# Performance work log

Hardware: AMD Instinct MI355X
Metric: run time of the kernel (lower is better)

Reference implementation:

```python
import jax, jax.numpy as jnp
import numpy as np

# ---- static config (mirrors module init / config constants) ----
STATE_DIM = 512
D_H = 2048
INPUT_DIM = 1024
N_QUBITS = 6
N_VQC_LAYERS = 3
MSD = 128                 # mamba_state_dim (last dim of padded state)
PAD_SLICES = 16           # padded slice count in h_padded
MIN_T = 1e-6              # control_limits.min_value
REL_STEP = 0.1            # control_limits.hardware_relative_step
ABS_STEP = 1e-4           # control_limits.hardware_absolute_step
MAX_T = 0.05              # control_limits.max_value
DIM = 2 ** N_QUBITS

# qubit 0 = most significant bit (matches reshape-based gate application)
_BITS = ((np.arange(DIM)[:, None] >> np.arange(N_QUBITS)[None, ::-1]) & 1).astype(np.float32)
_sign = np.ones(DIM, np.float32)
for k in range(N_QUBITS):  # ring CZ entanglement
    k2 = (k + 1) % N_QUBITS
    _sign *= 1.0 - 2.0 * _BITS[:, k] * _BITS[:, k2]
CZ_SIGN = jnp.asarray(_sign)
Z_OBS = jnp.asarray((1.0 - 2.0 * _BITS).mean(axis=1))  # mean <Z_k> observable weights


def _apply_ry(state, ang, k):
    # state: [B, 2^n] real statevector; ang: [B] rotation angle on qubit k
    B = state.shape[0]
    s = state.reshape(B, 2 ** k, 2, 2 ** (N_QUBITS - k - 1))
    c = jnp.cos(ang / 2)[:, None, None]
    si = jnp.sin(ang / 2)[:, None, None]
    a0, a1 = s[:, :, 0, :], s[:, :, 1, :]
    out = jnp.stack([c * a0 - si * a1, si * a0 + c * a1], axis=2)
    return out.reshape(B, DIM)


def _vqc(feats, enc_W, enc_b, thetas):
    # EvolutionTimeVQCLayer: angle-encode features, layered RY + ring CZ, mean-Z expectation
    B = feats.shape[0]
    angles = feats @ enc_W + enc_b  # [B, n_qubits]
    state = jnp.zeros((B, DIM), feats.dtype).at[:, 0].set(1.0)
    for k in range(N_QUBITS):
        state = _apply_ry(state, angles[:, k], k)
    for l in range(N_VQC_LAYERS):
        for k in range(N_QUBITS):
            state = _apply_ry(state, jnp.broadcast_to(thetas[l, k], (B,)), k)
        state = state * CZ_SIGN[None, :]
    return (state * state) @ Z_OBS  # [B]


def _hamiltonian(q, p, x, W1, b1, W2, b2, W3, b3):
    z = jnp.concatenate([q, p, x], axis=-1)          # [B, 2*S + D]
    h1 = jnp.tanh(z @ W1 + b1)
    h2 = jnp.tanh(h1 @ W2 + b2)
    return (h2 @ W3)[:, 0] + b3                       # [B] scalar energy per sample


def setup_inputs() -> dict:
    key = jax.random.key(0)
    ks = jax.random.split(key, 12)
    def glorot(k, shape):
        std = np.sqrt(2.0 / (shape[0] + shape[-1]))
        return jax.random.normal(k, shape, jnp.float32) * std
    B = 2048
    h_in = 2 * STATE_DIM + INPUT_DIM
    gen_in = INPUT_DIM + 2 * STATE_DIM
    return {
        'x': jax.random.normal(ks[0], (B, INPUT_DIM), jnp.float32),
        'h_padded': jax.random.normal(ks[1], (B, PAD_SLICES, MSD), jnp.float32),
        'aux_padded': jnp.zeros((B, PAD_SLICES, MSD), jnp.float32),
        'W1': glorot(ks[2], (h_in, D_H)), 'b1': jnp.zeros((D_H,), jnp.float32),
        'W2': glorot(ks[3], (D_H, D_H)), 'b2': jnp.zeros((D_H,), jnp.float32),
        'W3': glorot(ks[4], (D_H, 1)), 'b3': jnp.zeros((), jnp.float32),
        'W_out': glorot(ks[5], (2 * STATE_DIM, INPUT_DIM)),
        'b_out': jnp.zeros((INPUT_DIM,), jnp.float32),
        'enc_W': glorot(ks[6], (gen_in, N_QUBITS)) * 0.1,
        'enc_b': jnp.zeros((N_QUBITS,), jnp.float32),
        'thetas': jax.random.normal(ks[7], (N_VQC_LAYERS, N_QUBITS), jnp.float32) * 0.1,
        'gain': jnp.asarray(0.1, jnp.float32),
        'shift': jnp.asarray(7.0, jnp.float32),
        'cap_param': jnp.asarray(0.02, jnp.float32),
        'time_bias': jnp.asarray(0.0005, jnp.float32),
        'last_stable': jnp.asarray(0.0005, jnp.float32),
    }


def reference(x, h_padded, aux_padded, W1, b1, W2, b2, W3, b3, W_out, b_out,
              enc_W, enc_b, thetas, gain, shift, cap_param, time_bias, last_stable):
    B = x.shape[0]
    total = 2 * STATE_DIM
    num_slices = total // MSD
    # unpack phase-space state from padded mamba-shaped state
    unpacked = h_padded[:, :num_slices, :].reshape(B, total)
    q_t, p_t = jnp.split(unpacked, 2, axis=-1)

    # ---- evolution-time generation via VQC ----
    ctrl = jnp.concatenate([x, q_t, p_t], axis=-1)
    samples = _vqc(ctrl, enc_W, enc_b, thetas)                       # [B]
    soft_gain = jax.nn.softplus(gain)
    soft_shift = jax.nn.softplus(shift)
    adjusted = jax.nn.softplus(soft_gain * samples - soft_shift)
    raw = jnp.mean(adjusted) + time_bias
    cap = jnp.maximum(jax.nn.softplus(cap_param), 1e-6)
    evo = cap * jax.nn.sigmoid(raw / cap)
    evo = jnp.where(jnp.isfinite(evo), evo, cap * jax.nn.sigmoid(time_bias / cap))
    prev = jnp.maximum(last_stable, MIN_T)
    cand = jnp.maximum(evo, MIN_T)
    max_step = jnp.maximum(prev * REL_STEP, ABS_STEP)
    cand = jnp.minimum(cand, prev + max_step)
    cand = jnp.minimum(cand, MAX_T)
    dt = jnp.where(jnp.isfinite(cand), cand, prev)                   # scalar

    # ---- fused HNN symplectic (leapfrog) step ----
    def H_sum(q, p):
        return _hamiltonian(q, p, x, W1, b1, W2, b2, W3, b3).sum()
    grad_qp = jax.grad(H_sum, argnums=(0, 1))
    dHdq0, _ = grad_qp(q_t, p_t)
    p_half = p_t - 0.5 * dt * dHdq0
    _, dHdp_h = grad_qp(q_t, p_half)
    q_next = q_t + dt * dHdp_h
    dHdq_n, _ = grad_qp(q_next, p_half)
    p_next = p_half - 0.5 * dt * dHdq_n

    out = jnp.concatenate([q_next, p_next], axis=-1) @ W_out + b_out  # [B, INPUT_DIM]

    # repack state into padded mamba layout
    new_slices = jnp.concatenate([q_next, p_next], axis=-1).reshape(B, num_slices, MSD)
    pad = jnp.zeros((B, PAD_SLICES - num_slices, MSD), out.dtype)
    h_next = jnp.concatenate([new_slices, pad], axis=1)
    return out, h_next
```

## Files before the change

### kernel.cpp

```cpp
#include <hip/hip_runtime.h>
#include <math.h>

#define NB 2048
#define ZD 2048
#define SD 512
#define NELEM_Z (NB * ZD)
#define MB_ (1024 * 1024)

typedef float f32x4 __attribute__((ext_vector_type(4)));
typedef __bf16 bf16x8 __attribute__((ext_vector_type(8)));
typedef __bf16 bf16x4 __attribute__((ext_vector_type(4)));
typedef int i32x4 __attribute__((ext_vector_type(4)));
typedef int i32x8 __attribute__((ext_vector_type(8)));
typedef long long i64;

__device__ __forceinline__ float softplus_f(float x) {
  if (x > 20.f) return x;
  if (x < -20.f) return expf(x);
  return log1pf(expf(x));
}

__device__ __forceinline__ void gload_lds16(const __bf16* g, __bf16* l) {
  __builtin_amdgcn_global_load_lds(
      (__attribute__((address_space(1))) void*)(g),
      (__attribute__((address_space(3))) void*)(l), 16, 0, 0);
}

__device__ __forceinline__ int pack_fp8x4(float a, float b, float c, float d) {
  int p = __builtin_amdgcn_cvt_pk_fp8_f32(a, b, 0, false);
  p = __builtin_amdgcn_cvt_pk_fp8_f32(c, d, p, true);
  return p;
}
__device__ __forceinline__ float fp8_to_f32(unsigned char b) {
  return __builtin_amdgcn_cvt_f32_fp8((int)b, 0);
}

__global__ __launch_bounds__(256) void build_z_kernel(
    const float* __restrict__ x,
    const float* __restrict__ h_padded,
    const float* __restrict__ enc_W,
    const float* __restrict__ enc_b,
    float* __restrict__ z,
    __bf16* __restrict__ zb,
    unsigned char* __restrict__ zf8,
    float* __restrict__ angles,
    float* __restrict__ acc) {
  int b = blockIdx.x;
  int tid = threadIdx.x;
  if (b == 0 && tid == 0) acc[0] = 0.f;
  int lane = tid & 63, w = tid >> 6;
  __shared__ float red[4][6];

  float pa[6] = {0.f, 0.f, 0.f, 0.f, 0.f, 0.f};
#pragma unroll
  for (int cc = 0; cc < 2; cc++) {
    int c = cc * 256 + tid;
    int i = c * 4;
    f32x4 v = (i < 1024) ? ((const f32x4*)(h_padded + (size_t)b * 2048))[c]
                         : ((const f32x4*)(x + (size_t)b * 1024))[c - 256];
    size_t zi = (size_t)b * 512 + c;
    ((f32x4*)z)[zi] = v;
    bf16x4 o;
    o[0] = (__bf16)v[0]; o[1] = (__bf16)v[1];
    o[2] = (__bf16)v[2]; o[3] = (__bf16)v[3];
    ((bf16x4*)zb)[zi] = o;
    ((int*)zf8)[zi] = pack_fp8x4(v[0], v[1], v[2], v[3]);
    int cj = (i < 1024) ? (1024 + i) : (i - 1024);
#pragma unroll
    for (int e = 0; e < 4; e++) {
      const float* wp = enc_W + (size_t)(cj + e) * 6;
#pragma unroll
      for (int k = 0; k < 6; k++) pa[k] += v[e] * wp[k];
    }
  }
#pragma unroll
  for (int k = 0; k < 6; k++)
    for (int off = 32; off > 0; off >>= 1) pa[k] += __shfl_down(pa[k], off, 64);
  if (lane == 0) {
#pragma unroll
    for (int k = 0; k < 6; k++) red[w][k] = pa[k];
  }
  __syncthreads();
  if (tid < 6)
    angles[b * 6 + tid] =
        red[0][tid] + red[1][tid] + red[2][tid] + red[3][tid] + enc_b[tid];
}

__global__ void prep_w(const float* __restrict__ in,
                       __bf16* __restrict__ outT, int R, int C) {
  __shared__ float tile[32][33];
  int bx = blockIdx.x * 32, by = blockIdx.y * 32;
  int tx = threadIdx.x, ty = threadIdx.y;
  for (int r = ty; r < 32; r += 8)
    tile[r][tx] = in[(size_t)(by + r) * C + bx + tx];
  __syncthreads();
  for (int r = ty; r < 32; r += 8)
    outT[(size_t)(bx + r) * R + by + tx] = (__bf16)tile[tx][r];
}

__global__ void prep_w8(const float* __restrict__ in,
                        unsigned char* __restrict__ outN,
                        unsigned char* __restrict__ outT, int R, int C) {
  __shared__ float tile[32][33];
  int bx = blockIdx.x * 32, by = blockIdx.y * 32;
  int tx = threadIdx.x, ty = threadIdx.y;
  for (int r = ty; r < 32; r += 8) {
    float v = in[(size_t)(by + r) * C + bx + tx] * 16.f;
    tile[r][tx] = v;
    int p = __builtin_amdgcn_cvt_pk_fp8_f32(v, v, 0, false);
    outN[(size_t)(by + r) * C + bx + tx] = (unsigned char)(p & 0xff);
  }
  __syncthreads();
  for (int r = ty; r < 32; r += 8) {
    float v = tile[tx][r];
    int p = __builtin_amdgcn_cvt_pk_fp8_f32(v, v, 0, false);
    outT[(size_t)(bx + r) * R + by + tx] = (unsigned char)(p & 0xff);
  }
}

__global__ __launch_bounds__(64) void sim_kernel(
    const float* __restrict__ angles,
    const float* __restrict__ thetas,
    const float* __restrict__ gain,
    const float* __restrict__ shift,
    float* __restrict__ acc) {
  int row = blockIdx.x * 64 + threadIdx.x;
  const float* a = angles + row * 6;

  float s[64];
#pragma unroll
  for (int i = 0; i < 64; i++) s[i] = 0.f;
  s[0] = 1.f;

#pragma unroll
  for (int k = 0; k < 6; k++) {
    float half = 0.5f * a[k];
    float c = cosf(half), si = sinf(half);
    int m = 1 << (5 - k);
#pragma unroll
    for (int i = 0; i < 64; i++) {
      if ((i & m) == 0) {
        float a0 = s[i], a1 = s[i | m];
        s[i] = c * a0 - si * a1;
        s[i | m] = si * a0 + c * a1;
      }
    }
  }
#pragma unroll
  for (int l = 0; l < 3; l++) {
#pragma unroll
    for (int k = 0; k < 6; k++) {
      float half = 0.5f * thetas[l * 6 + k];
      float c = cosf(half), si = sinf(half);
      int m = 1 << (5 - k);
#pragma unroll
      for (int i = 0; i < 64; i++) {
        if ((i & m) == 0) {
          float a0 = s[i], a1 = s[i | m];
          s[i] = c * a0 - si * a1;
          s[i | m] = si * a0 + c * a1;
        }
      }
    }
#pragma unroll
    for (int i = 0; i < 64; i++) {
      int rot = ((i << 1) | (i >> 5)) & 63;
      if (__popc(i & rot) & 1) s[i] = -s[i];
    }
  }

  float val = 0.f;
#pragma unroll
  for (int i = 0; i < 64; i++) {
    float zo = (6.f - 2.f * (float)__popc(i)) * (1.f / 6.f);
    val += s[i] * s[i] * zo;
  }
  float sg = softplus_f(gain[0]);
  float ss = softplus_f(shift[0]);
  float adj = softplus_f(sg * val - ss);
  for (int off = 32; off > 0; off >>= 1) adj += __shfl_down(adj, off, 64);
  if (threadIdx.x == 0) atomicAdd(acc, adj);
}

__global__ void dt_kernel(const float* __restrict__ acc,
                          const float* __restrict__ cap_param,
                          const float* __restrict__ time_bias,
                          const float* __restrict__ last_stable,
                          float* __restrict__ dt_out) {
  float raw = acc[0] * (1.f / (float)NB) + time_bias[0];
  float cap = fmaxf(softplus_f(cap_param[0]), 1e-6f);
  float evo = cap / (1.f + expf(-raw / cap));
  if (!isfinite(evo)) evo = cap / (1.f + expf(-time_bias[0] / cap));
  float prev = fmaxf(last_stable[0], 1e-6f);
  float cand = fmaxf(evo, 1e-6f);
  float max_step = fmaxf(prev * 0.1f, 1e-4f);
  cand = fminf(cand, prev + max_step);
  cand = fminf(cand, 0.05f);
  dt_out[0] = isfinite(cand) ? cand : prev;
}

template <int EPI>
__global__ __launch_bounds__(256, 2) void mfma_gemm8(
    const unsigned char* __restrict__ A, int lda,
    const unsigned char* __restrict__ Bt, int ldb,
    void* __restrict__ Cv, int ldc,
    const float* __restrict__ bias,
    const float* __restrict__ w3,
    const unsigned char* __restrict__ aux, int ldaux,
    int Kslice) {
  __shared__ __align__(16) unsigned char sA[2][128 * 128];
  __shared__ __align__(16) unsigned char sB[2][64 * 128];

  const int tid = threadIdx.x;
  const int lane = tid & 63;
  const int w = tid >> 6;
  const int wm = w & 1, wn = w >> 1;
  const int row0 = blockIdx.y * 128;
  const int col0 = blockIdx.x * 64;
  const int koff = blockIdx.z * Kslice;

  const unsigned char* gA[4]; int wA[4];
  const unsigned char* gB[2]; int wB[2];
#pragma unroll
  for (int i = 0; i < 4; i++) {
    int c = i * 256 + tid;
    int m = c >> 3, s = c & 7;
    gA[i] = A + (size_t)(row0 + m) * lda + koff + s * 16;
    wA[i] = m * 128 + ((s ^ (m & 7)) << 4);
  }
#pragma unroll
  for (int i = 0; i < 2; i++) {
    int c = i * 256 + tid;
    int m = c >> 3, s = c & 7;
    gB[i] = Bt + (size_t)(col0 + m) * ldb + koff + s * 16;
    wB[i] = m * 128 + ((s ^ (m & 7)) << 4);
  }

  const int q = lane >> 4, r = lane & 15;
  int aoff[4][2], boff[2][2];
#pragma unroll
  for (int i = 0; i < 4; i++) {
    int ma = wm * 64 + i * 16 + r;
#pragma unroll
    for (int H = 0; H < 2; H++)
      aoff[i][H] = ma * 128 + (((2 * q + H) ^ (ma & 7)) << 4);
  }
#pragma unroll
  for (int j = 0; j < 2; j++) {
    int mb = wn * 32 + j * 16 + r;
#pragma unroll
    for (int H = 0; H < 2; H++)
      boff[j][H] = mb * 128 + (((2 * q + H) ^ (mb & 7)) << 4);
  }

  f32x4 acc[4][2] = {};
  f32x4 rA[4], rB[2];

#pragma unroll
  for (int i = 0; i < 4; i++) rA[i] = *(const f32x4*)gA[i];
#pragma unroll
  for (int i = 0; i < 2; i++) rB[i] = *(const f32x4*)gB[i];
#pragma unroll
  for (int i = 0; i < 4; i++) *(f32x4*)(&sA[0][0] + wA[i]) = rA[i];
#pragma unroll
  for (int i = 0; i < 2; i++) *(f32x4*)(&sB[0][0] + wB[i]) = rB[i];
  __syncthreads();

  int cur = 0;
  for (int k0 = 0; k0 < Kslice; k0 += 128) {
    const bool more = (k0 + 128 < Kslice);
    if (more) {
#pragma unroll
      for (int i = 0; i < 4; i++) rA[i] = *(const f32x4*)(gA[i] + k0 + 128);
#pragma unroll
      for (int i = 0; i < 2; i++) rB[i] = *(const f32x4*)(gB[i] + k0 + 128);
    }

    const unsigned char* bA = &sA[cur][0];
    const unsigned char* bB = &sB[cur][0];
    i32x8 af[4], bfr[2];
#pragma unroll
    for (int i = 0; i < 4; i++) {
      i32x4 lo = *(const i32x4*)(bA + aoff[i][0]);
      i32x4 hi = *(const i32x4*)(bA + aoff[i][1]);
      af[i] = __builtin_shufflevector(lo, hi, 0, 1, 2, 3, 4, 5, 6, 7);
    }
#pragma unroll
    for (int j = 0; j < 2; j++) {
      i32x4 lo = *(const i32x4*)(bB + boff[j][0]);
      i32x4 hi = *(const i32x4*)(bB + boff[j][1]);
      bfr[j] = __builtin_shufflevector(lo, hi, 0, 1, 2, 3, 4, 5, 6, 7);
    }
#pragma unroll
    for (int i = 0; i < 4; i++)
#pragma unroll
      for (int j = 0; j < 2; j++)
        acc[i][j] = __builtin_amdgcn_mfma_scale_f32_16x16x128_f8f6f4(
            af[i], bfr[j], acc[i][j], 0 , 0 ,
            0, 0x7F7F7F7F, 0, 0x7F7F7F7F);

    if (more) {
      unsigned char* nA = &sA[cur ^ 1][0];
      unsigned char* nB = &sB[cur ^ 1][0];
#pragma unroll
      for (int i = 0; i < 4; i++) *(f32x4*)(nA + wA[i]) = rA[i];
#pragma unroll
      for (int i = 0; i < 2; i++) *(f32x4*)(nB + wB[i]) = rB[i];
    }
    __syncthreads();
    cur ^= 1;
  }

  float* Cf = (float*)Cv;
  unsigned char* C8 = (unsigned char*)Cv;
  float* Pz = Cf + (size_t)blockIdx.z * (size_t)gridDim.y * 128 * ldc;

#pragma unroll
  for (int i = 0; i < 4; i++) {
    int rowb = row0 + wm * 64 + i * 16 + q * 4;
#pragma unroll
    for (int j = 0; j < 2; j++) {
      int col = col0 + wn * 32 + j * 16 + r;
      if (EPI == 0) {
#pragma unroll
        for (int g = 0; g < 4; g++)
          Pz[(size_t)(rowb + g) * ldc + col] = acc[i][j][g];
      } else {
        float o[4];
#pragma unroll
        for (int g = 0; g < 4; g++) {
          float v = acc[i][j][g] * 0.0625f;
          if (EPI == 1) {
            o[g] = tanhf(v + bias[col]);
          } else if (EPI == 2) {
            float t = tanhf(v + bias[col]);
            o[g] = 32.f * (1.f - t * t) * w3[col];
          } else {
            float h = fp8_to_f32(aux[(size_t)(rowb + g) * ldaux + col]);
            o[g] = v * (1.f - h * h);
          }
        }
        int p = pack_fp8x4(o[0], o[1], o[2], o[3]);
#pragma unroll
        for (int g = 0; g < 4; g++)
          C8[(size_t)(rowb + g) * ldc + col] =
              (unsigned char)((p >> (8 * g)) & 0xff);
      }
    }
  }
}

__global__ __launch_bounds__(256, 2) void mfma_gemm_bf16(
    const __bf16* __restrict__ A, int lda,
    const __bf16* __restrict__ Bt, int ldb,
    float* __restrict__ P, int ldc,
    int Kslice) {
  __shared__ __bf16 sA[2][128 * 64];
  __shared__ __bf16 sB[2][64 * 64];

  const int tid = threadIdx.x;
  const int lane = tid & 63;
  const int w = tid >> 6;
  const int wm = w & 1, wn = w >> 1;
  const int row0 = blockIdx.y * 128;
  const int col0 = blockIdx.x * 64;
  const int koff = blockIdx.z * Kslice;

  const __bf16* gA[4]; int lofA[4];
  const __bf16* gB[2]; int lofB[2];
#pragma unroll
  for (int i = 0; i < 4; i++) {
    int c = i * 256 + tid;
    int m = c >> 3, cc = c & 7;
    int o = cc ^ (m & 7);
    gA[i] = A + (size_t)(row0 + m) * lda + koff + o * 8;
    lofA[i] = c * 8;
  }
#pragma unroll
  for (int i = 0; i < 2; i++) {
    int c = i * 256 + tid;
    int m = c >> 3, cc = c & 7;
    int o = cc ^ (m & 7);
    gB[i] = Bt + (size_t)(col0 + m) * ldb + koff + o * 8;
    lofB[i] = c * 8;
  }

  const int q = lane >> 4, r = lane & 15;
  int aoff[4][2], boff[2][2];
#pragma unroll
  for (int i = 0; i < 4; i++) {
    int ma = wm * 64 + i * 16 + r;
#pragma unroll
    for (int h = 0; h < 2; h++)
      aoff[i][h] = (ma * 8 + ((h * 4 + q) ^ (ma & 7))) * 8;
  }
#pragma unroll
  for (int j = 0; j < 2; j++) {
    int mb = wn * 32 + j * 16 + r;
#pragma unroll
    for (int h = 0; h < 2; h++)
      boff[j][h] = (mb * 8 + ((h * 4 + q) ^ (mb & 7))) * 8;
  }

  f32x4 acc[4][2] = {};

#pragma unroll
  for (int i = 0; i < 4; i++) gload_lds16(gA[i], &sA[0][0] + lofA[i]);
#pragma unroll
  for (int i = 0; i < 2; i++) gload_lds16(gB[i], &sB[0][0] + lofB[i]);

  int cur = 0;
  for (int k0 = 0; k0 < Kslice; k0 += 64) {
    __syncthreads();
    if (k0 + 64 < Kslice) {
      int nxt = cur ^ 1;
#pragma unroll
      for (int i = 0; i < 4; i++)
        gload_lds16(gA[i] + k0 + 64, &sA[nxt][0] + lofA[i]);
#pragma unroll
      for (int i = 0; i < 2; i++)
        gload_lds16(gB[i] + k0 + 64, &sB[nxt][0] + lofB[i]);
    }
#pragma unroll
    for (int h = 0; h < 2; h++) {
      bf16x8 af[4], bfr[2];
#pragma unroll
      for (int i = 0; i < 4; i++)
        af[i] = *(const bf16x8*)(&sA[cur][0] + aoff[i][h]);
#pragma unroll
      for (int j = 0; j < 2; j++)
        bfr[j] = *(const bf16x8*)(&sB[cur][0] + boff[j][h]);
#pragma unroll
      for (int i = 0; i < 4; i++)
#pragma unroll
        for (int j = 0; j < 2; j++)
          acc[i][j] = __builtin_amdgcn_mfma_f32_16x16x32_bf16(af[i], bfr[j],
                                                              acc[i][j], 0, 0, 0);
    }
    cur ^= 1;
  }

  float* Pz = P + (size_t)blockIdx.z * (size_t)gridDim.y * 128 * ldc;
#pragma unroll
  for (int i = 0; i < 4; i++) {
    int rowb = row0 + wm * 64 + i * 16 + q * 4;
#pragma unroll
    for (int j = 0; j < 2; j++) {
      int col = col0 + wn * 32 + j * 16 + r;
#pragma unroll
      for (int g = 0; g < 4; g++)
        Pz[(size_t)(rowb + g) * ldc + col] = acc[i][j][g];
    }
  }
}

__global__ void update_kernel(float* __restrict__ z, __bf16* __restrict__ zb,
                              unsigned char* __restrict__ zf8,
                              const float* __restrict__ gp,
                              const float* __restrict__ dt,
                              float coef, int off) {
  int t = blockIdx.x * blockDim.x + threadIdx.x;
  int b = t >> 7;
  int j4 = t & 127;
  const f32x4* g4 = (const f32x4*)gp;
  constexpr int STRIDE = NB * SD / 4;
  f32x4 g = g4[t] + g4[t + STRIDE] + g4[t + 2 * STRIDE] + g4[t + 3 * STRIDE];
  int zi4 = (b * ZD + off) / 4 + j4;
  f32x4 v = ((f32x4*)z)[zi4];
  float s = coef * dt[0] * (1.f / 512.f);
  v[0] += s * g[0]; v[1] += s * g[1]; v[2] += s * g[2]; v[3] += s * g[3];
  ((f32x4*)z)[zi4] = v;
  bf16x4 o;
  o[0] = (__bf16)v[0]; o[1] = (__bf16)v[1];
  o[2] = (__bf16)v[2]; o[3] = (__bf16)v[3];
  ((bf16x4*)zb)[zi4] = o;
  ((int*)zf8)[zi4] = pack_fp8x4(v[0], v[1], v[2], v[3]);
}

__global__ void wout_reduce(const float* __restrict__ gp,
                            const float* __restrict__ b_out,
                            float* __restrict__ out) {
  int t = blockIdx.x * blockDim.x + threadIdx.x;
  constexpr int S = NB * 1024 / 4;
  const f32x4* g4 = (const f32x4*)gp;
  f32x4 v = g4[t] + g4[t + S];
  f32x4 bb = ((const f32x4*)b_out)[t & 255];
  v[0] += bb[0]; v[1] += bb[1]; v[2] += bb[2]; v[3] += bb[3];
  ((f32x4*)out)[t] = v;
}

__global__ void hnext_kernel(const float* __restrict__ z,
                             float* __restrict__ out) {
  int t = blockIdx.x * blockDim.x + threadIdx.x;
  int i4 = t & 511;
  f32x4 zero = {0.f, 0.f, 0.f, 0.f};
  ((f32x4*)out)[t] = (i4 < 256) ? ((const f32x4*)z)[t] : zero;
}

extern "C" void kernel_launch(void* const* d_in, const int* in_sizes, int n_in,
                              void* d_out, int out_size, void* d_ws,
                              size_t ws_size, hipStream_t stream) {
  const float* x        = (const float*)d_in[0];
  const float* h_padded = (const float*)d_in[1];
  const float* W1    = (const float*)d_in[3];
  const float* b1    = (const float*)d_in[4];
  const float* W2    = (const float*)d_in[5];
  const float* b2    = (const float*)d_in[6];
  const float* W3    = (const float*)d_in[7];
  const float* W_out = (const float*)d_in[9];
  const float* b_out = (const float*)d_in[10];
  const float* enc_W = (const float*)d_in[11];
  const float* enc_b = (const float*)d_in[12];
  const float* thetas = (const float*)d_in[13];
  const float* gain   = (const float*)d_in[14];
  const float* shift  = (const float*)d_in[15];
  const float* cap_p  = (const float*)d_in[16];
  const float* t_bias = (const float*)d_in[17];
  const float* l_stab = (const float*)d_in[18];

  float* out_mat  = (float*)d_out;
  float* out_hnxt = (float*)d_out + NB * 1024;

  char* base = (char*)d_ws;
  float* z      = (float*)(base);
  float* part   = (float*)(base + 16 * MB_);
  __bf16* zb    = (__bf16*)(base + 32 * MB_);
  __bf16* Wot   = (__bf16*)(base + 40 * MB_);
  float* angl   = (float*)(base + 42 * MB_);
  float* accp   = (float*)(base + 42 * MB_ + 65536);
  float* dtp    = accp + 1;
  unsigned char* zf8  = (unsigned char*)(base + 43 * MB_);
  unsigned char* h1_8 = zf8 + (size_t)NELEM_Z;
  unsigned char* g2_8 = h1_8 + (size_t)NELEM_Z;
  unsigned char* g1_8 = g2_8 + (size_t)NELEM_Z;
  unsigned char* W1n8 = g1_8 + (size_t)NELEM_Z;
  unsigned char* W1t8 = W1n8 + (size_t)NELEM_Z;
  unsigned char* W2n8 = W1t8 + (size_t)NELEM_Z;
  unsigned char* W2t8 = W2n8 + (size_t)NELEM_Z;

  dim3 thr256(256);
  dim3 thrT(32, 8);

  prep_w8<<<dim3(64, 64), thrT, 0, stream>>>(W1, W1n8, W1t8, ZD, ZD);
  prep_w8<<<dim3(64, 64), thrT, 0, stream>>>(W2, W2n8, W2t8, ZD, ZD);
  prep_w<<<dim3(32, 32), thrT, 0, stream>>>(W_out, Wot, 1024, 1024);

  build_z_kernel<<<dim3(NB), thr256, 0, stream>>>(x, h_padded, enc_W, enc_b, z,
                                                  zb, zf8, angl, accp);
  sim_kernel<<<dim3(NB / 64), dim3(64), 0, stream>>>(angl, thetas, gain, shift,
                                                     accp);
  dt_kernel<<<dim3(1), dim3(1), 0, stream>>>(accp, cap_p, t_bias, l_stab, dtp);

  const int   j0r[3]  = {0, 512, 0};
  const int   offs[3] = {512, 0, 512};
  const float coef[3] = {-0.5f, 1.0f, -0.5f};

  dim3 gridSq(32, 16, 1);
  dim3 gridGr(8, 16, 4);

  for (int i = 0; i < 3; i++) {
    mfma_gemm8<1><<<gridSq, thr256, 0, stream>>>(
        zf8, ZD, W1t8, ZD, h1_8, ZD, b1, nullptr, nullptr, 0, ZD);
    mfma_gemm8<2><<<gridSq, thr256, 0, stream>>>(
        h1_8, ZD, W2t8, ZD, g2_8, ZD, b2, W3, nullptr, 0, ZD);
    mfma_gemm8<3><<<gridSq, thr256, 0, stream>>>(
        g2_8, ZD, W2n8, ZD, g1_8, ZD, nullptr, nullptr, h1_8, ZD, ZD);
    mfma_gemm8<0><<<gridGr, thr256, 0, stream>>>(
        g1_8, ZD, W1n8 + (size_t)j0r[i] * ZD, ZD, part, SD, nullptr, nullptr,
        nullptr, 0, 512);
    update_kernel<<<dim3(NB * SD / 4 / 256), thr256, 0, stream>>>(
        z, zb, zf8, part, dtp, coef[i], offs[i]);
  }

  mfma_gemm_bf16<<<dim3(16, 16, 2), thr256, 0, stream>>>(zb, ZD, Wot, 1024,
                                                         part, 1024, 512);
  wout_reduce<<<dim3(NB * 1024 / 4 / 256), thr256, 0, stream>>>(part, b_out,
                                                                out_mat);

  hnext_kernel<<<dim3(NELEM_Z / 4 / 256), thr256, 0, stream>>>(z, out_hnxt);
}
```

Baseline: 474.2 us.

## Parallelize VQC statevector simulation across wavefront lanes using shuffles

The quantum circuit simulation moves from one thread per sample, which keeps a 64-entry statevector in registers, to one wavefront per sample with one amplitude per lane. Each RY gate becomes a lane-xor shuffle plus an FMA, and CZ signs and Z weights are computed per lane. The expectation value is reduced with xor shuffles and four waves per block combine through shared memory before a single atomic add. This removes register pressure and serial work per thread and raises parallelism from 32 blocks to 512, at the cost of many cross-lane shuffles and every lane redundantly computing the gate trig.

```diff
diff --git a/kernel.cpp b/kernel.cpp
--- a/kernel.cpp
+++ b/kernel.cpp
@@ -118,68 +118,59 @@
   }
 }
 
-__global__ __launch_bounds__(64) void sim_kernel(
+__global__ __launch_bounds__(256) void sim_kernel(
     const float* __restrict__ angles,
     const float* __restrict__ thetas,
     const float* __restrict__ gain,
     const float* __restrict__ shift,
     float* __restrict__ acc) {
-  int row = blockIdx.x * 64 + threadIdx.x;
+  const int lane = threadIdx.x & 63;
+  const int wv = threadIdx.x >> 6;
+  const int row = blockIdx.x * 4 + wv;
   const float* a = angles + row * 6;
 
-  float s[64];
-#pragma unroll
-  for (int i = 0; i < 64; i++) s[i] = 0.f;
-  s[0] = 1.f;
+  const int rot = ((lane << 1) | (lane >> 5)) & 63;
+  const float czs = (__popc(lane & rot) & 1) ? -1.f : 1.f;
+  const float zo = (6.f - 2.f * (float)__popc(lane)) * (1.f / 6.f);
+
+  float s = (lane == 0) ? 1.f : 0.f;
 
 #pragma unroll
   for (int k = 0; k < 6; k++) {
+    const int m = 1 << (5 - k);
     float half = 0.5f * a[k];
     float c = cosf(half), si = sinf(half);
-    int m = 1 << (5 - k);
-#pragma unroll
-    for (int i = 0; i < 64; i++) {
-      if ((i & m) == 0) {
-        float a0 = s[i], a1 = s[i | m];
-        s[i] = c * a0 - si * a1;
-        s[i | m] = si * a0 + c * a1;
-      }
-    }
+    float t = __shfl_xor(s, m, 64);
+    float ssi = (lane & m) ? si : -si;
+    s = fmaf(c, s, ssi * t);
   }
 #pragma unroll
   for (int l = 0; l < 3; l++) {
 #pragma unroll
     for (int k = 0; k < 6; k++) {
+      const int m = 1 << (5 - k);
       float half = 0.5f * thetas[l * 6 + k];
       float c = cosf(half), si = sinf(half);
-      int m = 1 << (5 - k);
-#pragma unroll
-      for (int i = 0; i < 64; i++) {
-        if ((i & m) == 0) {
-          float a0 = s[i], a1 = s[i | m];
-          s[i] = c * a0 - si * a1;
-          s[i | m] = si * a0 + c * a1;
-        }
-      }
-    }
-#pragma unroll
-    for (int i = 0; i < 64; i++) {
-      int rot = ((i << 1) | (i >> 5)) & 63;
-      if (__popc(i & rot) & 1) s[i] = -s[i];
-    }
-  }
-
-  float val = 0.f;
-#pragma unroll
-  for (int i = 0; i < 64; i++) {
-    float zo = (6.f - 2.f * (float)__popc(i)) * (1.f / 6.f);
-    val += s[i] * s[i] * zo;
-  }
+      float t = __shfl_xor(s, m, 64);
+      float ssi = (lane & m) ? si : -si;
+      s = fmaf(c, s, ssi * t);
+    }
+    s *= czs;
+  }
+
+  float val = s * s * zo;
+#pragma unroll
+  for (int off = 32; off > 0; off >>= 1) val += __shfl_xor(val, off, 64);
+
   float sg = softplus_f(gain[0]);
   float ss = softplus_f(shift[0]);
   float adj = softplus_f(sg * val - ss);
-  for (int off = 32; off > 0; off >>= 1) adj += __shfl_down(adj, off, 64);
-  if (threadIdx.x == 0) atomicAdd(acc, adj);
+
+  __shared__ float red[4];
+  if (lane == 0) red[wv] = adj;
+  __syncthreads();
+  if (threadIdx.x == 0)
+    atomicAdd(acc, red[0] + red[1] + red[2] + red[3]);
 }
 
 __global__ void dt_kernel(const float* __restrict__ acc,
@@ -547,8 +538,8 @@
 
   build_z_kernel<<<dim3(NB), thr256, 0, stream>>>(x, h_padded, enc_W, enc_b, z,
                                                   zb, zf8, angl, accp);
-  sim_kernel<<<dim3(NB / 64), dim3(64), 0, stream>>>(angl, thetas, gain, shift,
-                                                     accp);
+  sim_kernel<<<dim3(NB / 4), thr256, 0, stream>>>(angl, thetas, gain, shift,
+                                                  accp);
   dt_kernel<<<dim3(1), dim3(1), 0, stream>>>(accp, cap_p, t_bias, l_stab, dtp);
 
   const int   j0r[3]  = {0, 512, 0};
```

Measured after the change: 434.6 us. -8.4%, faster.
